# Kernel tuning notes

Hardware: AMD Instinct MI355X
Metric: run time of the kernel (lower is better)

The kernel has to match this reference:

```python
import jax, jax.numpy as jnp
import numpy as np

BETA = 0.5  # hard-negative concentration (module default)


def _l2norm(x, axis):
    return x / jnp.linalg.norm(x, axis=axis, keepdims=True)


def setup_inputs() -> dict:
    key = jax.random.key(0)
    k1, k2, k3 = jax.random.split(key, 3)
    B, V, D = 4096, 2, 512
    features = jax.random.normal(k1, (B, V, D), dtype=jnp.float32)
    out_1 = jax.random.normal(k2, (B, D), dtype=jnp.float32)
    out_2 = jax.random.normal(k3, (B, D), dtype=jnp.float32)
    indexes = jnp.arange(B, dtype=jnp.int64)
    return {"features": features, "out_1": out_1, "out_2": out_2, "indexes": indexes}


def reference(features, out_1, out_2, indexes):
    # features is normalized in the original forward but unused afterwards
    _ = _l2norm(features, axis=2)

    o1 = _l2norm(out_1, axis=-1)
    o2 = _l2norm(out_2, axis=-1)
    out = jnp.concatenate([o1, o2], axis=0)            # [2B, D]
    label = jnp.concatenate([indexes, indexes], axis=0)  # [2B]
    batch = label.shape[0]

    # cost = exp(2 * out @ out.T), [2B, 2B]
    cost = jnp.exp(2.0 * jnp.einsum('id,jd->ij', out, out))

    pos_full = (label[:, None] == label[None, :]).astype(cost.dtype)
    neg_index = 1.0 - pos_full
    pos_index = pos_full - jnp.eye(batch, dtype=cost.dtype)

    pos = pos_index * cost
    neg = neg_index * cost

    # importance weights: neg_index * exp(beta * log(neg)) == neg_index * neg**beta
    imp = jax.lax.stop_gradient(neg_index * jnp.power(neg, BETA))
    neg_exp_sum = (imp * neg).sum(axis=-1) / imp.sum(axis=-1)  # [2B]

    denom = pos + (batch - 2) * neg_exp_sum[:, None]
    ratio = pos / denom

    mask = pos_index > 0
    safe_ratio = jnp.where(mask, ratio, 1.0)
    nce = -(jnp.log(safe_ratio) * pos_index).sum() / pos_index.sum()
    return nce
```

## Files before the change

kernel.cpp:

```cpp
#include <hip/hip_runtime.h>
#include <stdint.h>

#define BHALF 4096
#define NROWS 8192
#define DDIM  512
#define KNEG  8190.0f

#define BM   128
#define BK   32
#define NK   (DDIM / BK)
#define NTIL 64
#define TBLK (NTIL * (NTIL + 1) / 2)
#define FABLK 256

typedef short v8s __attribute__((ext_vector_type(8)));
typedef float v4f __attribute__((ext_vector_type(4)));

static __device__ inline float bf2f(uint32_t u) {
    union { uint32_t i; float f; } c; c.i = u << 16; return c.f;
}
static __device__ inline uint32_t f2bf(float f) {
    union { float f; uint32_t i; } c; c.f = f;
    return (c.i + 0x7fffu + ((c.i >> 16) & 1u)) >> 16;
}

#define GLL16(gp, lp)                                                         \
    __builtin_amdgcn_global_load_lds(                                         \
        (__attribute__((address_space(1))) void*)(gp),                        \
        (__attribute__((address_space(3))) void*)(lp), 16, 0, 0)


__global__ __launch_bounds__(256) void rownorm_cvt_kernel(
    const void* __restrict__ o1, const void* __restrict__ o2,
    float* __restrict__ rn, uint16_t* __restrict__ cvt2)
{
    int wave = threadIdx.x >> 6, lane = threadIdx.x & 63;
    int row = blockIdx.x * 4 + wave;

    uint32_t w = ((const uint32_t*)o1)[lane * 977 + 13];
    uint32_t e = (w >> 7) & 0xFFu;
    int bad = (e < 100u || e > 140u) ? 1 : 0;
    #pragma unroll
    for (int m = 32; m; m >>= 1) bad += __shfl_xor(bad, m);

    float ss;
    uint4 pack;
    if (bad <= 16) {
        const uint16_t* s = (row < BHALF)
            ? (const uint16_t*)o1 + (size_t)row * DDIM
            : (const uint16_t*)o2 + (size_t)(row - BHALF) * DDIM;
        pack = ((const uint4*)s)[lane];
        float a0 = bf2f(pack.x & 0xffffu), a1 = bf2f(pack.x >> 16);
        float a2 = bf2f(pack.y & 0xffffu), a3 = bf2f(pack.y >> 16);
        float a4 = bf2f(pack.z & 0xffffu), a5 = bf2f(pack.z >> 16);
        float a6 = bf2f(pack.w & 0xffffu), a7 = bf2f(pack.w >> 16);
        ss = a0*a0 + a1*a1 + a2*a2 + a3*a3 + a4*a4 + a5*a5 + a6*a6 + a7*a7;
    } else {
        const float* s = (row < BHALF)
            ? (const float*)o1 + (size_t)row * DDIM
            : (const float*)o2 + (size_t)(row - BHALF) * DDIM;
        float4 a = ((const float4*)s)[2 * lane];
        float4 b = ((const float4*)s)[2 * lane + 1];
        ss = a.x*a.x + a.y*a.y + a.z*a.z + a.w*a.w
           + b.x*b.x + b.y*b.y + b.z*b.z + b.w*b.w;
        pack.x = f2bf(a.x) | (f2bf(a.y) << 16);
        pack.y = f2bf(a.z) | (f2bf(a.w) << 16);
        pack.z = f2bf(b.x) | (f2bf(b.y) << 16);
        pack.w = f2bf(b.z) | (f2bf(b.w) << 16);
    }
    size_t byteoff = (size_t)(row >> 4) * 16384 + (size_t)lane * 256
                   + (size_t)(row & 15) * 16;
    *(uint4*)((char*)cvt2 + byteoff) = pack;

    #pragma unroll
    for (int m = 32; m; m >>= 1) ss += __shfl_xor(ss, m);
    if (lane == 0) rn[row] = rsqrtf(ss);
}

__global__ __launch_bounds__(256, 4) void SupCon_hcl_49323404427556_kernel(
    const uint16_t* __restrict__ cvt2, const float* __restrict__ rn,
    float* __restrict__ pden, float* __restrict__ pnum, float* __restrict__ cpos)
{
    __shared__ alignas(16) char sbuf[2][16384];
    __shared__ float rnA[BM], rnB[BM];
    float (*s_dr)[2] = (float(*)[2])(&sbuf[0][0]);
    float (*s_nr)[2] = (float(*)[2])(&sbuf[0][1024]);
    float (*s_dc)[2] = (float(*)[2])(&sbuf[0][2048]);
    float (*s_nc)[2] = (float(*)[2])(&sbuf[0][3072]);

    int tid  = threadIdx.x;
    int wave = tid >> 6, lane = tid & 63;
    int quad = lane >> 4, l16 = lane & 15;
    int wrow = (wave >> 1) * 64, wcol = (wave & 1) * 64;

    int b = blockIdx.x;
    int t = (b & 7) * (TBLK / 8) + (b >> 3);

    int bi = (int)(64.5f - sqrtf(64.5f * 64.5f - 2.0f * (float)t));
    while (bi > 0 && (64 * bi - (bi * (bi - 1)) / 2) > t) --bi;
    while ((64 * (bi + 1) - ((bi + 1) * bi) / 2) <= t) ++bi;
    int bj = bi + (t - (64 * bi - (bi * (bi - 1)) / 2));
    int i0 = bi * BM, j0 = bj * BM;
    bool diag = (bi == bj);
    bool partner = (bj == bi + 32) && (bi < 32);
    bool plain = !diag && !partner;

    if (tid < BM) rnA[tid] = rn[i0 + tid];
    else          rnB[tid - BM] = rn[j0 + (tid - BM)];

    const char* cb = (const char*)cvt2;
    const char* gA0 = cb + ((size_t)(i0 >> 4) + 2 * wave) * 16384 + (size_t)lane * 16;
    const char* gA1 = gA0 + 16384;
    const char* gB0 = cb + ((size_t)(j0 >> 4) + 2 * wave) * 16384 + (size_t)lane * 16;
    const char* gB1 = gB0 + 16384;
    int dA0 = (2 * wave) * 1024, dA1 = dA0 + 1024;
    int dB0 = 8192 + dA0,        dB1 = dB0 + 1024;

    GLL16(gA0, &sbuf[0][dA0]);
    GLL16(gA1, &sbuf[0][dA1]);
    GLL16(gB0, &sbuf[0][dB0]);
    GLL16(gB1, &sbuf[0][dB1]);

    v4f acc[4][4];
    v4f z = {0.f, 0.f, 0.f, 0.f};
    #pragma unroll
    for (int a = 0; a < 4; ++a)
        #pragma unroll
        for (int bb = 0; bb < 4; ++bb) acc[a][bb] = z;

    int rgA = wrow >> 4, rgB = wcol >> 4;

    #pragma unroll
    for (int kb = 0; kb < NK; ++kb) {
        if (kb < NK - 1) {
            char* wb = &sbuf[(kb + 1) & 1][0];
            GLL16(gA0 + (kb + 1) * 1024, wb + dA0);
            GLL16(gA1 + (kb + 1) * 1024, wb + dA1);
            GLL16(gB0 + (kb + 1) * 1024, wb + dB0);
            GLL16(gB1 + (kb + 1) * 1024, wb + dB1);
            asm volatile("s_waitcnt vmcnt(4)" ::: "memory");
        } else {
            asm volatile("s_waitcnt vmcnt(0)" ::: "memory");
        }
        __builtin_amdgcn_s_barrier();
        __builtin_amdgcn_sched_barrier(0);

        const char* rb = &sbuf[kb & 1][0];
        v8s af[4], bfr[4];
        #pragma unroll
        for (int tt = 0; tt < 4; ++tt) {
            af[tt]  = *(const v8s*)(rb + (rgA + tt) * 1024 + lane * 16);
            bfr[tt] = *(const v8s*)(rb + 8192 + (rgB + tt) * 1024 + lane * 16);
        }
        __builtin_amdgcn_s_setprio(1);
        #pragma unroll
        for (int mt = 0; mt < 4; ++mt)
            #pragma unroll
            for (int nt = 0; nt < 4; ++nt)
                acc[mt][nt] = __builtin_amdgcn_mfma_f32_16x16x32_bf16(
                    af[mt], bfr[nt], acc[mt][nt], 0, 0, 0);
        __builtin_amdgcn_s_setprio(0);
        __builtin_amdgcn_s_barrier();
    }

    if (plain) {
        float rjv[4];
        #pragma unroll
        for (int nt = 0; nt < 4; ++nt) rjv[nt] = rnB[wcol + 16 * nt + l16];

        float pd[16], pn[16], cdv[4], cnv[4];
        #pragma unroll
        for (int k = 0; k < 16; ++k) { pd[k] = 0.f; pn[k] = 0.f; }
        #pragma unroll
        for (int nt = 0; nt < 4; ++nt) { cdv[nt] = 0.f; cnv[nt] = 0.f; }

        #pragma unroll
        for (int mt = 0; mt < 4; ++mt) {
            #pragma unroll
            for (int r = 0; r < 4; ++r) {
                float ri = rnA[wrow + 16 * mt + quad * 4 + r];
                #pragma unroll
                for (int nt = 0; nt < 4; ++nt) {
                    float e  = __expf(acc[mt][nt][r] * ri * rjv[nt]);
                    float e3 = e * e * e;
                    pd[mt * 4 + r] += e;   pn[mt * 4 + r] += e3;
                    cdv[nt]        += e;   cnv[nt]        += e3;
                }
            }
        }

        #define BSTEP(arr, n, bit)                                            \
            _Pragma("unroll")                                                 \
            for (int p = 0; p < (n); ++p) {                                   \
                float mine = (l16 & (bit)) ? arr[2*p+1] : arr[2*p];           \
                float send = (l16 & (bit)) ? arr[2*p]   : arr[2*p+1];         \
                arr[p] = mine + __shfl_xor(send, (bit));                      \
            }
        BSTEP(pd, 8, 1) BSTEP(pd, 4, 2) BSTEP(pd, 2, 4) BSTEP(pd, 1, 8)
        BSTEP(pn, 8, 1) BSTEP(pn, 4, 2) BSTEP(pn, 2, 4) BSTEP(pn, 1, 8)
        #undef BSTEP

        int rowk = wrow + 16 * (l16 >> 2) + quad * 4 + (l16 & 3);
        s_dr[rowk][wcol >> 6] = pd[0];
        s_nr[rowk][wcol >> 6] = pn[0];

        #pragma unroll
        for (int nt = 0; nt < 4; ++nt) {
            float cd = cdv[nt] + __shfl_xor(cdv[nt], 16);
            cd += __shfl_xor(cd, 32);
            float cn = cnv[nt] + __shfl_xor(cnv[nt], 16);
            cn += __shfl_xor(cn, 32);
            if (quad == 0) {
                s_dc[wcol + 16 * nt + l16][wrow >> 6] = cd;
                s_nc[wcol + 16 * nt + l16][wrow >> 6] = cn;
            }
        }
    } else {
        #pragma unroll
        for (int mt = 0; mt < 4; ++mt) {
            #pragma unroll
            for (int nt = 0; nt < 4; ++nt) {
                float rj = rnB[wcol + 16 * nt + l16];
                #pragma unroll
                for (int r = 0; r < 4; ++r) {
                    float ri = rnA[wrow + 16 * mt + quad * 4 + r];
                    acc[mt][nt][r] = __expf(acc[mt][nt][r] * ri * rj);
                }
            }
        }

        #pragma unroll
        for (int mt = 0; mt < 4; ++mt) {
            #pragma unroll
            for (int r = 0; r < 4; ++r) {
                int gil = wrow + 16 * mt + quad * 4 + r;
                int gi = i0 + gil;
                int pr = gi ^ BHALF;
                float pdv = 0.f, pnv = 0.f;
                #pragma unroll
                for (int nt = 0; nt < 4; ++nt) {
                    int gj = j0 + wcol + 16 * nt + l16;
                    float e = acc[mt][nt][r];
                    if (gj == pr) cpos[gi] = e * e;
                    if (gj != gi && gj != pr) { pdv += e; pnv += e * e * e; }
                }
                #pragma unroll
                for (int m = 1; m < 16; m <<= 1) {
                    pdv += __shfl_xor(pdv, m);
                    pnv += __shfl_xor(pnv, m);
                }
                if (l16 == 0) { s_dr[gil][wcol >> 6] = pdv; s_nr[gil][wcol >> 6] = pnv; }
            }
        }

        if (!diag) {
            #pragma unroll
            for (int nt = 0; nt < 4; ++nt) {
                int gjl = wcol + 16 * nt + l16;
                int gj = j0 + gjl;
                int pj = gj ^ BHALF;
                float cd = 0.f, cn = 0.f;
                #pragma unroll
                for (int mt = 0; mt < 4; ++mt) {
                    #pragma unroll
                    for (int r = 0; r < 4; ++r) {
                        int gi = i0 + wrow + 16 * mt + quad * 4 + r;
                        float e = acc[mt][nt][r];
                        if (gi == pj) cpos[gj] = e * e;
                        else { cd += e; cn += e * e * e; }
                    }
                }
                cd += __shfl_xor(cd, 16); cn += __shfl_xor(cn, 16);
                cd += __shfl_xor(cd, 32); cn += __shfl_xor(cn, 32);
                if (quad == 0) { s_dc[gjl][wrow >> 6] = cd; s_nc[gjl][wrow >> 6] = cn; }
            }
        }
    }

    __syncthreads();
    if (tid < BM) {
        pden[(size_t)bj * NROWS + i0 + tid] = s_dr[tid][0] + s_dr[tid][1];
        pnum[(size_t)bj * NROWS + i0 + tid] = s_nr[tid][0] + s_nr[tid][1];
        if (!diag) {
            pden[(size_t)bi * NROWS + j0 + tid] = s_dc[tid][0] + s_dc[tid][1];
            pnum[(size_t)bi * NROWS + j0 + tid] = s_nc[tid][0] + s_nc[tid][1];
        }
    }
}

__global__ __launch_bounds__(256) void finalizeA_kernel(
    const float* __restrict__ pden, const float* __restrict__ pnum,
    const float* __restrict__ cpos, float* __restrict__ bpart)
{
    int b = blockIdx.x, t = threadIdx.x;
    int r = b * 32 + (t & 31);
    int c = t >> 5;
    float pd = 0.f, pn = 0.f;
    #pragma unroll
    for (int i = 0; i < 8; ++i) {
        int x = c + 8 * i;
        pd += pden[(size_t)x * NROWS + r];
        pn += pnum[(size_t)x * NROWS + r];
    }
    pd += __shfl_xor(pd, 32);
    pn += __shfl_xor(pn, 32);

    __shared__ float sd[4][32], sn[4][32];
    int wave = t >> 6, lane = t & 63;
    if (lane < 32) { sd[wave][lane] = pd; sn[wave][lane] = pn; }
    __syncthreads();

    float s = 0.f;
    if (t < 32) {
        float d = sd[0][t] + sd[1][t] + sd[2][t] + sd[3][t];
        float n = sn[0][t] + sn[1][t] + sn[2][t] + sn[3][t];
        s = logf(1.0f + KNEG * (n / d) / cpos[b * 32 + t]);
    }
    if (t < 64) {
        #pragma unroll
        for (int m = 32; m; m >>= 1) s += __shfl_xor(s, m);
        if (t == 0) bpart[b] = s;
    }
}

__global__ __launch_bounds__(256) void finalizeB_kernel(
    const float* __restrict__ bpart, float* __restrict__ out)
{
    int t = threadIdx.x;
    float s = bpart[t];
    #pragma unroll
    for (int m = 32; m; m >>= 1) s += __shfl_xor(s, m);
    __shared__ float wsum[4];
    if ((t & 63) == 0) wsum[t >> 6] = s;
    __syncthreads();
    if (t == 0) out[0] = (wsum[0] + wsum[1] + wsum[2] + wsum[3]) / (float)NROWS;
}

extern "C" void kernel_launch(void* const* d_in, const int* in_sizes, int n_in,
                              void* d_out, int out_size, void* d_ws, size_t ws_size,
                              hipStream_t stream)
{
    const void* o1 = d_in[1];
    const void* o2 = d_in[2];

    uint16_t* cvt2 = (uint16_t*)d_ws;
    float* pden = (float*)(cvt2 + (size_t)NROWS * DDIM);
    float* pnum = pden + (size_t)NTIL * NROWS;
    float* rn   = pnum + (size_t)NTIL * NROWS;
    float* cpos = rn + NROWS;
    float* bpart= cpos + NROWS;

    rownorm_cvt_kernel<<<NROWS / 4, 256, 0, stream>>>(o1, o2, rn, cvt2);
    SupCon_hcl_49323404427556_kernel<<<TBLK, 256, 0, stream>>>(cvt2, rn, pden, pnum, cpos);
    finalizeA_kernel<<<FABLK, 256, 0, stream>>>(pden, pnum, cpos, bpart);
    finalizeB_kernel<<<1, 256, 0, stream>>>(bpart, (float*)d_out);
}
```

Before: 151.0 us.

## Enlarge symmetric Gram tiles to 256x256 with 512-thread blocks

Doubles the block tile of the upper-triangular Gram computation from 128 to 256 rows and columns, using 8 waves per block each owning a 128x64 sub-tile. This halves the number of tile rows, which cuts global/LDS reloads per output and the number of partial-sum columns the finalize pass must reduce. In exchange the block grid shrinks to 528 blocks, per-thread accumulator and register pressure doubles, and LDS use per block grows, all of which can lower occupancy and load balance on the GPU.

```diff
diff --git a/kernel.cpp b/kernel.cpp
--- a/kernel.cpp
+++ b/kernel.cpp
@@ -6,10 +6,10 @@
 #define DDIM  512
 #define KNEG  8190.0f
 
-#define BM   128
+#define BM   256
 #define BK   32
 #define NK   (DDIM / BK)
-#define NTIL 64
+#define NTIL 32
 #define TBLK (NTIL * (NTIL + 1) / 2)
 #define FABLK 256
 
@@ -77,58 +77,57 @@
     if (lane == 0) rn[row] = rsqrtf(ss);
 }
 
-__global__ __launch_bounds__(256, 4) void SupCon_hcl_49323404427556_kernel(
+__global__ __launch_bounds__(512) void SupCon_hcl_49323404427556_kernel(
     const uint16_t* __restrict__ cvt2, const float* __restrict__ rn,
     float* __restrict__ pden, float* __restrict__ pnum, float* __restrict__ cpos)
 {
-    __shared__ alignas(16) char sbuf[2][16384];
+    __shared__ alignas(16) char sbuf[2][32768];
     __shared__ float rnA[BM], rnB[BM];
-    float (*s_dr)[2] = (float(*)[2])(&sbuf[0][0]);
-    float (*s_nr)[2] = (float(*)[2])(&sbuf[0][1024]);
-    float (*s_dc)[2] = (float(*)[2])(&sbuf[0][2048]);
-    float (*s_nc)[2] = (float(*)[2])(&sbuf[0][3072]);
+    float (*s_dr)[4] = (float(*)[4])(&sbuf[0][0]);
+    float (*s_nr)[4] = (float(*)[4])(&sbuf[0][4096]);
+    float (*s_dc)[2] = (float(*)[2])(&sbuf[0][8192]);
+    float (*s_nc)[2] = (float(*)[2])(&sbuf[0][10240]);
 
     int tid  = threadIdx.x;
     int wave = tid >> 6, lane = tid & 63;
     int quad = lane >> 4, l16 = lane & 15;
-    int wrow = (wave >> 1) * 64, wcol = (wave & 1) * 64;
+    int wr = wave >> 2, wc = wave & 3;
+    int wrow = wr * 128, wcol = wc * 64;
 
     int b = blockIdx.x;
     int t = (b & 7) * (TBLK / 8) + (b >> 3);
 
-    int bi = (int)(64.5f - sqrtf(64.5f * 64.5f - 2.0f * (float)t));
-    while (bi > 0 && (64 * bi - (bi * (bi - 1)) / 2) > t) --bi;
-    while ((64 * (bi + 1) - ((bi + 1) * bi) / 2) <= t) ++bi;
-    int bj = bi + (t - (64 * bi - (bi * (bi - 1)) / 2));
+    int bi = (int)(32.5f - sqrtf(32.5f * 32.5f - 2.0f * (float)t));
+    while (bi > 0 && (32 * bi - (bi * (bi - 1)) / 2) > t) --bi;
+    while ((32 * (bi + 1) - ((bi + 1) * bi) / 2) <= t) ++bi;
+    int bj = bi + (t - (32 * bi - (bi * (bi - 1)) / 2));
     int i0 = bi * BM, j0 = bj * BM;
     bool diag = (bi == bj);
-    bool partner = (bj == bi + 32) && (bi < 32);
+    bool partner = (bj == bi + 16);
     bool plain = !diag && !partner;
 
     if (tid < BM) rnA[tid] = rn[i0 + tid];
     else          rnB[tid - BM] = rn[j0 + (tid - BM)];
 
     const char* cb = (const char*)cvt2;
-    const char* gA0 = cb + ((size_t)(i0 >> 4) + 2 * wave) * 16384 + (size_t)lane * 16;
+    const char* gA0 = cb + ((size_t)bi * 16 + 2 * wave) * 16384 + (size_t)lane * 16;
     const char* gA1 = gA0 + 16384;
-    const char* gB0 = cb + ((size_t)(j0 >> 4) + 2 * wave) * 16384 + (size_t)lane * 16;
+    const char* gB0 = cb + ((size_t)bj * 16 + 2 * wave) * 16384 + (size_t)lane * 16;
     const char* gB1 = gB0 + 16384;
-    int dA0 = (2 * wave) * 1024, dA1 = dA0 + 1024;
-    int dB0 = 8192 + dA0,        dB1 = dB0 + 1024;
+    int dA0 = 2 * wave * 1024, dA1 = dA0 + 1024;
+    int dB0 = 16384 + dA0,     dB1 = dB0 + 1024;
 
     GLL16(gA0, &sbuf[0][dA0]);
     GLL16(gA1, &sbuf[0][dA1]);
     GLL16(gB0, &sbuf[0][dB0]);
     GLL16(gB1, &sbuf[0][dB1]);
 
-    v4f acc[4][4];
+    v4f acc[8][4];
     v4f z = {0.f, 0.f, 0.f, 0.f};
     #pragma unroll
-    for (int a = 0; a < 4; ++a)
+    for (int a = 0; a < 8; ++a)
         #pragma unroll
         for (int bb = 0; bb < 4; ++bb) acc[a][bb] = z;
-
-    int rgA = wrow >> 4, rgB = wcol >> 4;
 
     #pragma unroll
     for (int kb = 0; kb < NK; ++kb) {
@@ -146,15 +145,16 @@
         __builtin_amdgcn_sched_barrier(0);
 
         const char* rb = &sbuf[kb & 1][0];
-        v8s af[4], bfr[4];
-        #pragma unroll
-        for (int tt = 0; tt < 4; ++tt) {
-            af[tt]  = *(const v8s*)(rb + (rgA + tt) * 1024 + lane * 16);
-            bfr[tt] = *(const v8s*)(rb + 8192 + (rgB + tt) * 1024 + lane * 16);
-        }
+        v8s af[8], bfr[4];
+        #pragma unroll
+        for (int tt = 0; tt < 8; ++tt)
+            af[tt]  = *(const v8s*)(rb + (wr * 8 + tt) * 1024 + lane * 16);
+        #pragma unroll
+        for (int tt = 0; tt < 4; ++tt)
+            bfr[tt] = *(const v8s*)(rb + 16384 + (wc * 4 + tt) * 1024 + lane * 16);
         __builtin_amdgcn_s_setprio(1);
         #pragma unroll
-        for (int mt = 0; mt < 4; ++mt)
+        for (int mt = 0; mt < 8; ++mt)
             #pragma unroll
             for (int nt = 0; nt < 4; ++nt)
                 acc[mt][nt] = __builtin_amdgcn_mfma_f32_16x16x32_bf16(
@@ -168,14 +168,14 @@
         #pragma unroll
         for (int nt = 0; nt < 4; ++nt) rjv[nt] = rnB[wcol + 16 * nt + l16];
 
-        float pd[16], pn[16], cdv[4], cnv[4];
-        #pragma unroll
-        for (int k = 0; k < 16; ++k) { pd[k] = 0.f; pn[k] = 0.f; }
+        float pd[32], pn[32], cdv[4], cnv[4];
+        #pragma unroll
+        for (int k = 0; k < 32; ++k) { pd[k] = 0.f; pn[k] = 0.f; }
         #pragma unroll
         for (int nt = 0; nt < 4; ++nt) { cdv[nt] = 0.f; cnv[nt] = 0.f; }
 
         #pragma unroll
-        for (int mt = 0; mt < 4; ++mt) {
+        for (int mt = 0; mt < 8; ++mt) {
             #pragma unroll
             for (int r = 0; r < 4; ++r) {
                 float ri = rnA[wrow + 16 * mt + quad * 4 + r];
@@ -196,13 +196,16 @@
                 float send = (l16 & (bit)) ? arr[2*p]   : arr[2*p+1];         \
                 arr[p] = mine + __shfl_xor(send, (bit));                      \
             }
-        BSTEP(pd, 8, 1) BSTEP(pd, 4, 2) BSTEP(pd, 2, 4) BSTEP(pd, 1, 8)
-        BSTEP(pn, 8, 1) BSTEP(pn, 4, 2) BSTEP(pn, 2, 4) BSTEP(pn, 1, 8)
+        BSTEP(pd, 16, 1) BSTEP(pd, 8, 2) BSTEP(pd, 4, 4) BSTEP(pd, 2, 8)
+        BSTEP(pn, 16, 1) BSTEP(pn, 8, 2) BSTEP(pn, 4, 4) BSTEP(pn, 2, 8)
         #undef BSTEP
 
-        int rowk = wrow + 16 * (l16 >> 2) + quad * 4 + (l16 & 3);
-        s_dr[rowk][wcol >> 6] = pd[0];
-        s_nr[rowk][wcol >> 6] = pn[0];
+        #pragma unroll
+        for (int p = 0; p < 2; ++p) {
+            int rowk = wrow + 16 * ((p << 2) | (l16 >> 2)) + quad * 4 + (l16 & 3);
+            s_dr[rowk][wc] = pd[p];
+            s_nr[rowk][wc] = pn[p];
+        }
 
         #pragma unroll
         for (int nt = 0; nt < 4; ++nt) {
@@ -211,13 +214,13 @@
             float cn = cnv[nt] + __shfl_xor(cnv[nt], 16);
             cn += __shfl_xor(cn, 32);
             if (quad == 0) {
-                s_dc[wcol + 16 * nt + l16][wrow >> 6] = cd;
-                s_nc[wcol + 16 * nt + l16][wrow >> 6] = cn;
+                s_dc[wcol + 16 * nt + l16][wr] = cd;
+                s_nc[wcol + 16 * nt + l16][wr] = cn;
             }
         }
     } else {
         #pragma unroll
-        for (int mt = 0; mt < 4; ++mt) {
+        for (int mt = 0; mt < 8; ++mt) {
             #pragma unroll
             for (int nt = 0; nt < 4; ++nt) {
                 float rj = rnB[wcol + 16 * nt + l16];
@@ -230,7 +233,7 @@
         }
 
         #pragma unroll
-        for (int mt = 0; mt < 4; ++mt) {
+        for (int mt = 0; mt < 8; ++mt) {
             #pragma unroll
             for (int r = 0; r < 4; ++r) {
                 int gil = wrow + 16 * mt + quad * 4 + r;
@@ -249,7 +252,7 @@
                     pdv += __shfl_xor(pdv, m);
                     pnv += __shfl_xor(pnv, m);
                 }
-                if (l16 == 0) { s_dr[gil][wcol >> 6] = pdv; s_nr[gil][wcol >> 6] = pnv; }
+                if (l16 == 0) { s_dr[gil][wc] = pdv; s_nr[gil][wc] = pnv; }
             }
         }
 
@@ -261,7 +264,7 @@
                 int pj = gj ^ BHALF;
                 float cd = 0.f, cn = 0.f;
                 #pragma unroll
-                for (int mt = 0; mt < 4; ++mt) {
+                for (int mt = 0; mt < 8; ++mt) {
                     #pragma unroll
                     for (int r = 0; r < 4; ++r) {
                         int gi = i0 + wrow + 16 * mt + quad * 4 + r;
@@ -272,15 +275,20 @@
                 }
                 cd += __shfl_xor(cd, 16); cn += __shfl_xor(cn, 16);
                 cd += __shfl_xor(cd, 32); cn += __shfl_xor(cn, 32);
-                if (quad == 0) { s_dc[gjl][wrow >> 6] = cd; s_nc[gjl][wrow >> 6] = cn; }
-            }
+                if (quad == 0) { s_dc[gjl][wr] = cd; s_nc[gjl][wr] = cn; }
+            }
+        } else {
+            if (tid < BM) { s_dc[tid][0] = 0.f; s_dc[tid][1] = 0.f;
+                            s_nc[tid][0] = 0.f; s_nc[tid][1] = 0.f; }
         }
     }
 
     __syncthreads();
     if (tid < BM) {
-        pden[(size_t)bj * NROWS + i0 + tid] = s_dr[tid][0] + s_dr[tid][1];
-        pnum[(size_t)bj * NROWS + i0 + tid] = s_nr[tid][0] + s_nr[tid][1];
+        pden[(size_t)bj * NROWS + i0 + tid]
+            = s_dr[tid][0] + s_dr[tid][1] + s_dr[tid][2] + s_dr[tid][3];
+        pnum[(size_t)bj * NROWS + i0 + tid]
+            = s_nr[tid][0] + s_nr[tid][1] + s_nr[tid][2] + s_nr[tid][3];
         if (!diag) {
             pden[(size_t)bi * NROWS + j0 + tid] = s_dc[tid][0] + s_dc[tid][1];
             pnum[(size_t)bi * NROWS + j0 + tid] = s_nc[tid][0] + s_nc[tid][1];
@@ -297,7 +305,7 @@
     int c = t >> 5;
     float pd = 0.f, pn = 0.f;
     #pragma unroll
-    for (int i = 0; i < 8; ++i) {
+    for (int i = 0; i < 4; ++i) {
         int x = c + 8 * i;
         pd += pden[(size_t)x * NROWS + r];
         pn += pnum[(size_t)x * NROWS + r];
@@ -351,7 +359,7 @@
     float* bpart= cpos + NROWS;
 
     rownorm_cvt_kernel<<<NROWS / 4, 256, 0, stream>>>(o1, o2, rn, cvt2);
-    SupCon_hcl_49323404427556_kernel<<<TBLK, 256, 0, stream>>>(cvt2, rn, pden, pnum, cpos);
+    SupCon_hcl_49323404427556_kernel<<<TBLK, 512, 0, stream>>>(cvt2, rn, pden, pnum, cpos);
     finalizeA_kernel<<<FABLK, 256, 0, stream>>>(pden, pnum, cpos, bpart);
     finalizeB_kernel<<<1, 256, 0, stream>>>(bpart, (float*)d_out);
 }
```

Result: slower. 183.7 us (+21.6%).
